# Performance work log

Hardware: AMD Instinct MI355X
Metric: run time of the kernel (lower is better)

## Reference

```python
import jax, jax.numpy as jnp
import numpy as np

B, S, D, H = 2, 2048, 4096, 32
HD = D // H  # 128
HALF = HD // 2  # 64


def setup_inputs() -> dict:
    key = jax.random.key(0)
    ks = jax.random.split(key, 6)
    scale = 1.0 / np.sqrt(D)
    x = jax.random.normal(ks[0], (B, S, D), jnp.float32)
    Wq = jax.random.normal(ks[1], (D, D), jnp.float32) * scale
    Wk = jax.random.normal(ks[2], (D, D), jnp.float32) * scale
    Wv = jax.random.normal(ks[3], (D, D), jnp.float32) * scale
    Wo = jax.random.normal(ks[4], (D, D), jnp.float32) * scale
    # Rotary frequencies: complex freqs of shape (S, HD//2) split into cos/sin
    inv_freq = 1.0 / (10000.0 ** (np.arange(0, HD, 2, dtype=np.float32) / HD))
    angles = np.outer(np.arange(S, dtype=np.float32), inv_freq)  # (S, HALF)
    freq_cos = jnp.asarray(np.cos(angles), jnp.float32)
    freq_sin = jnp.asarray(np.sin(angles), jnp.float32)
    # Additive causal mask (0 on/below diag, large-negative above)
    causal = jnp.tril(jnp.ones((S, S), jnp.bool_))
    mask = jnp.where(causal, 0.0, -1e9).astype(jnp.float32)
    return {"x": x, "Wq": Wq, "Wk": Wk, "Wv": Wv, "Wo": Wo,
            "freq_cos": freq_cos, "freq_sin": freq_sin, "mask": mask,
            "start_position": 0, "n_rep": 1}


def _apply_rope(t, freq_cos, freq_sin):
    # t: [B, S, H, HD]; complex multiply on interleaved (even, odd) pairs
    b, s, h, hd = t.shape
    tr = t.reshape(b, s, h, hd // 2, 2)
    a, c = tr[..., 0], tr[..., 1]
    cos = freq_cos[None, :, None, :]  # [1, S, 1, HALF]
    sin = freq_sin[None, :, None, :]
    out = jnp.stack([a * cos - c * sin, a * sin + c * cos], axis=-1)
    return out.reshape(b, s, h, hd)


def reference(x, Wq, Wk, Wv, Wo, freq_cos, freq_sin, mask, start_position, n_rep):
    b, s, _ = x.shape
    q = (x @ Wq).reshape(b, s, H, HD)
    k = (x @ Wk).reshape(b, s, H, HD)
    v = (x @ Wv).reshape(b, s, H, HD)
    q = _apply_rope(q, freq_cos, freq_sin)
    k = _apply_rope(k, freq_cos, freq_sin)
    if n_rep > 1:  # repeat_kv (identity when n_rep == 1)
        k = jnp.repeat(k, n_rep, axis=2)
        v = jnp.repeat(v, n_rep, axis=2)
    # KV-cache: with start_position=0 and s == max_sequence_length, the
    # cache slice [:, :start_position+s] equals the freshly written k/v.
    scores = jnp.einsum('bqhd,bkhd->bhqk', q, k) / jnp.sqrt(jnp.float32(HD))
    scores = scores + mask  # broadcast [S,S] over [B,H,S,S]
    weights = jax.nn.softmax(scores, axis=-1)
    out = jnp.einsum('bhqk,bkhd->bqhd', weights, v)
    out = out.reshape(b, s, H * HD)
    return out @ Wo
```

## Files before the change

### kernel.cpp

```cpp
#include <hip/hip_runtime.h>
#include <hip/hip_bf16.h>

#define DD 4096
#define MM 4096
#define SS 2048
#define HH 32
#define HDD 128
#define NT 64

typedef unsigned short u16;
typedef unsigned int u32;
typedef __attribute__((ext_vector_type(8))) __bf16 bf16x8;
typedef __attribute__((ext_vector_type(4))) float f32x4;
typedef __attribute__((ext_vector_type(4))) float float4v;
typedef __attribute__((ext_vector_type(8))) unsigned short ushort8;
typedef __attribute__((ext_vector_type(4))) unsigned int uint4v;

__device__ __forceinline__ u16 f2bf(float f) {
  union { float f; unsigned u; } v; v.f = f;
  unsigned u = v.u;
  return (u16)((u + 0x7fffu + ((u >> 16) & 1u)) >> 16);
}
__device__ __forceinline__ float bf2f(u16 s) {
  union { unsigned u; float f; } v; v.u = ((unsigned)s) << 16;
  return v.f;
}
__device__ __forceinline__ f32x4 zero4() { f32x4 z = {0.f, 0.f, 0.f, 0.f}; return z; }

__device__ __forceinline__ void gl_lds16(const u16* g, u16* l) {
  __builtin_amdgcn_global_load_lds((__attribute__((address_space(1))) void*)(g),
                                   (__attribute__((address_space(3))) void*)(l), 16, 0, 0);
}

__device__ __forceinline__ unsigned cvtpk(float lo, float hi) {
  unsigned r;
  asm("v_cvt_pk_bf16_f32 %0, %1, %2" : "=v"(r) : "v"(lo), "v"(hi));
  return r;
}
__device__ __forceinline__ u16 cvt1(float v) {
  unsigned r;
  asm("v_cvt_pk_bf16_f32 %0, %1, %1" : "=v"(r) : "v"(v));
  return (u16)r;
}
__device__ __forceinline__ float exp2a(float x) {
  float r;
  asm("v_exp_f32 %0, %1" : "=v"(r) : "v"(x));
  return r;
}

__global__ __launch_bounds__(256) void k_cvt(const float* __restrict__ in,
                                             u16* __restrict__ out, int n8) {
  int i = blockIdx.x * blockDim.x + threadIdx.x;
  if (i >= n8) return;
  size_t o = (size_t)i * 8;
  float4v a = *(const float4v*)(in + o);
  float4v b = *(const float4v*)(in + o + 4);
  ushort8 v;
  v[0] = f2bf(a[0]); v[1] = f2bf(a[1]); v[2] = f2bf(a[2]); v[3] = f2bf(a[3]);
  v[4] = f2bf(b[0]); v[5] = f2bf(b[1]); v[6] = f2bf(b[2]); v[7] = f2bf(b[3]);
  *(ushort8*)(out + o) = v;
}

__global__ __launch_bounds__(256) void k_wt(const float* __restrict__ W0,
                                            const float* __restrict__ W1,
                                            const float* __restrict__ W2,
                                            const float* __restrict__ W3,
                                            u16* __restrict__ out) {
  const float* W = blockIdx.z == 0 ? W0 : blockIdx.z == 1 ? W1 : blockIdx.z == 2 ? W2 : W3;
  u16* O = out + (size_t)blockIdx.z * DD * DD;
  __shared__ u16 t[64][66];
  int k0 = blockIdx.x * 64, n0 = blockIdx.y * 64;
  int tx = threadIdx.x, ty = threadIdx.y;
#pragma unroll
  for (int i = 0; i < 16; ++i) {
    int kk = ty + i * 4;
    t[tx][kk] = cvt1(W[(size_t)(k0 + kk) * DD + n0 + tx]);
  }
  __syncthreads();
  const int L = ty * 64 + tx;
  const int kx = L & 31, nb = L >> 5;
#pragma unroll
  for (int i = 0; i < 8; ++i) {
    int nn = nb + i * 8;
    u32 pk = *(const u32*)&t[nn][2 * kx];
    *(u32*)&O[(size_t)(n0 + nn) * DD + k0 + 2 * kx] = pk;
  }
}

#define MFMA16(QM, QN)                                                             \
  _Pragma("unroll") for (int kk = 0; kk < 2; ++kk)                                 \
  _Pragma("unroll") for (int mi = 0; mi < 4; ++mi)                                 \
  _Pragma("unroll") for (int ni = 0; ni < 2; ++ni)                                 \
      acc[(QM)*4 + mi][(QN)*2 + ni] = __builtin_amdgcn_mfma_f32_16x16x32_bf16(     \
          af[mi][kk], bf[(QN)*2 + ni][kk], acc[(QM)*4 + mi][(QN)*2 + ni], 0, 0, 0);

#define RDA(BB, QM)                                                                \
  _Pragma("unroll") for (int mi = 0; mi < 4; ++mi)                                 \
  _Pragma("unroll") for (int kk = 0; kk < 2; ++kk)                                 \
      af[mi][kk] = *(const bf16x8*)((const char*)&L[BB][0][0] +                    \
          ((abase + ((QM)*4 + mi) * 2048 + kk * 64) ^ xsw));

#define RDB(BB, QN)                                                                \
  _Pragma("unroll") for (int ni = 0; ni < 2; ++ni)                                 \
  _Pragma("unroll") for (int kk = 0; kk < 2; ++kk)                                 \
      bf[(QN)*2 + ni][kk] = *(const bf16x8*)((const char*)&L[BB][1][0] +           \
          ((bbase + ((QN)*2 + ni) * 2048 + kk * 64) ^ xsw));

#define BAR() __builtin_amdgcn_s_barrier()
#define LGKM0() asm volatile("s_waitcnt lgkmcnt(0)" ::: "memory")
#define PRIO1() __builtin_amdgcn_s_setprio(1)
#define PRIO0() __builtin_amdgcn_s_setprio(0)

template <int MODE>
__global__ __launch_bounds__(512, 2) void k_gemm(const u16* __restrict__ A,
                                                 const u16* __restrict__ Bt,
                                                 void* __restrict__ Cout) {
  __shared__ __align__(16) u16 L[2][2][16384];
  const int tid = threadIdx.x;
  const int wid = tid >> 6, lane = tid & 63;
  const int g = lane >> 4, li = lane & 15;
  const int wr = wid >> 2, wc = wid & 3;

  const int bid = blockIdx.x;
  const int sw = ((bid & 7) << 5) | (bid >> 3);
  const int brow = (sw >> 4) * 256, bcol = (sw & 15) * 256;

  const int xsw = (li & 7) << 4;
  const int abase = (wr * 128 + li) * 128 + g * 16;
  const int bbase = (wc * 64 + li) * 128 + g * 16;

  const int sxy = ((tid >> 3) & 7) << 3;
  const int scol = ((tid * 8) ^ sxy) & 63;
  const int srow0 = tid >> 3;

  auto STAGEH = [&](int t, int mat, int half) {
    if (t >= NT) return;
    const int bb2 = t & 1;
    const u16* G = mat ? Bt : A;
    const int rowbase = (mat ? bcol : brow) + half * 128;
    u16* Ld = &L[bb2][mat][half * 8192 + wid * 512];
    const u16* gsrc = G + (size_t)(rowbase + srow0) * DD + (t << 6) + scol;
    gl_lds16(gsrc, Ld);
    gl_lds16(gsrc + (size_t)64 * DD, Ld + 4096);
  };

  f32x4 acc[8][4];
#pragma unroll
  for (int m = 0; m < 8; ++m)
#pragma unroll
    for (int n = 0; n < 4; ++n) acc[m][n] = zero4();

  bf16x8 af[4][2], bf[4][2];

  STAGEH(0, 0, 0); STAGEH(0, 0, 1); STAGEH(0, 1, 0); STAGEH(0, 1, 1);
  STAGEH(1, 0, 0); STAGEH(1, 1, 0); STAGEH(1, 1, 1);
  asm volatile("s_waitcnt vmcnt(6)" ::: "memory");
  BAR();

  for (int kt = 0; kt < NT; ++kt) {
    const int bb = kt & 1;
    RDA(bb, 0); RDB(bb, 0);
    STAGEH(kt + 1, 0, 1);
    asm volatile("s_waitcnt lgkmcnt(8)" ::: "memory");
    BAR(); LGKM0();
    PRIO1(); MFMA16(0, 0); PRIO0();
    BAR();
    RDB(bb, 1);
    BAR(); LGKM0();
    PRIO1(); MFMA16(0, 1); PRIO0();
    BAR();
    RDA(bb, 1);
    STAGEH(kt + 2, 1, 0);
    BAR(); LGKM0();
    PRIO1(); MFMA16(1, 0); PRIO0();
    BAR();
    STAGEH(kt + 2, 1, 1);
    STAGEH(kt + 2, 0, 0);
    if (kt < NT - 2) {
      asm volatile("s_waitcnt vmcnt(6)" ::: "memory");
    } else {
      asm volatile("s_waitcnt vmcnt(0)" ::: "memory");
    }
    BAR(); LGKM0();
    PRIO1(); MFMA16(1, 1); PRIO0();
    BAR();
  }

#pragma unroll
  for (int m = 0; m < 8; ++m) {
#pragma unroll
    for (int n = 0; n < 4; ++n) {
#pragma unroll
      for (int r = 0; r < 4; ++r) {
        int row = brow + wr * 128 + m * 16 + g * 4 + r;
        int col = bcol + wc * 64 + n * 16 + li;
        float v = acc[m][n][r];
        if (MODE == 0) {
          ((u16*)Cout)[(size_t)row * DD + col] = cvt1(v);
        } else if (MODE == 1) {
          ((u16*)Cout)[((size_t)((row >> 11) << 12) + col) * SS + (row & 2047)] = cvt1(v);
        } else {
          ((float*)Cout)[(size_t)row * DD + col] = v;
        }
      }
    }
  }
}

__global__ __launch_bounds__(256) void k_rope(u16* __restrict__ Q, u16* __restrict__ Kp,
                                              const float* __restrict__ fc,
                                              const float* __restrict__ fs) {
  int idx = blockIdx.x * blockDim.x + threadIdx.x;
  const int n8 = MM * DD / 8;
  const float qsc = idx < n8 ? 0.08838834764831845f * 1.44269504088896340f : 1.0f;
  u16* T = idx < n8 ? Q : Kp;
  int i = idx < n8 ? idx : idx - n8;
  int m = i >> 9;
  int c = (i & 511) * 8;
  int s = m & (SS - 1);
  int i0 = (c & (HDD - 1)) >> 1;
  size_t o = (size_t)m * DD + c;
  ushort8 v = *(ushort8*)(T + o);
  float4v cs = *(const float4v*)(fc + s * 64 + i0);
  float4v sn = *(const float4v*)(fs + s * 64 + i0);
  ushort8 ov;
#pragma unroll
  for (int p = 0; p < 4; ++p) {
    float a = bf2f(v[2 * p]), cc = bf2f(v[2 * p + 1]);
    ov[2 * p]     = cvt1((a * cs[p] - cc * sn[p]) * qsc);
    ov[2 * p + 1] = cvt1((a * sn[p] + cc * cs[p]) * qsc);
  }
  *(ushort8*)(T + o) = ov;
}

__global__ __launch_bounds__(256) void k_attn(const u16* __restrict__ Q,
                                              const u16* __restrict__ K,
                                              const u16* __restrict__ VT,
                                              u16* __restrict__ O) {
  __shared__ __align__(16) u16 Kl[2][32 * 128];
  __shared__ __align__(16) u16 Vl[2][128 * 32];
  __shared__ __align__(16) u16 Pl[4][16 * 32];
  const int bh = blockIdx.x;
  const int qt = 31 - blockIdx.y;
  const int b = bh >> 5, h = bh & 31;
  const int tid = threadIdx.x, w = tid >> 6, lane = tid & 63;
  const int g = lane >> 4, li = lane & 15;

  const u16* Qbase = Q + ((size_t)(b * SS + qt * 64 + w * 16 + li)) * DD + h * HDD;
  const u16* Kbase = K + ((size_t)(b * SS)) * DD + h * HDD;
  const u16* Vbase = VT + ((size_t)bh) * HDD * SS;

  bf16x8 qf[4];
#pragma unroll
  for (int ks = 0; ks < 4; ++ks)
    qf[ks] = *(const bf16x8*)(Qbase + ks * 32 + g * 8);

  f32x4 oa[8];
#pragma unroll
  for (int f = 0; f < 8; ++f) oa[f] = zero4();
  float lrun = 0.f;
  const int wli = w * 16 + li;

  const int krow0 = w * 8 + (lane >> 4);
  const int ksg0 = (lane & 15) ^ (lane >> 4);
  const int ksg1 = (lane & 15) ^ (4 + (lane >> 4));
  const int vdr0 = w * 16 + (lane >> 2);
  const int va0 = (vdr0 * 64 + (lane & 3) * 16) ^ (((vdr0 >> 1) & 7) << 4);
  const int vdr1 = vdr0 + 64;
  const int va1 = (vdr1 * 64 + (lane & 3) * 16) ^ (((vdr1 >> 1) & 7) << 4);

  auto STAGE = [&](int t, int nb) {
    const u16* Kt = Kbase + (size_t)(t * 32) * DD;
    gl_lds16(Kt + (size_t)krow0 * DD + ksg0 * 8, &Kl[nb][(w * 8) * 128]);
    gl_lds16(Kt + (size_t)(krow0 + 4) * DD + ksg1 * 8, &Kl[nb][(w * 8 + 4) * 128]);
    const u16* Vt = Vbase + t * 32;
    gl_lds16(Vt + (size_t)(va0 >> 6) * SS + ((va0 >> 4) & 3) * 8, &Vl[nb][w * 512]);
    gl_lds16(Vt + (size_t)(va1 >> 6) * SS + ((va1 >> 4) & 3) * 8, &Vl[nb][2048 + w * 512]);
  };

  auto TILE = [&](int kt, int cb, int koff) __attribute__((always_inline)) {
    f32x4 sc[2];
    sc[0] = zero4(); sc[1] = zero4();
    PRIO1();
#pragma unroll
    for (int ks = 0; ks < 4; ++ks) {
#pragma unroll
      for (int ktg = 0; ktg < 2; ++ktg) {
        int kr = ktg * 16 + li;
        int off = (kr * 256 + (ks * 32 + g * 8) * 2) ^ ((kr & 7) << 4);
        bf16x8 kf = *(const bf16x8*)((const char*)Kl[cb] + off);
        sc[ktg] = __builtin_amdgcn_mfma_f32_16x16x32_bf16(kf, qf[ks], sc[ktg], 0, 0, 0);
      }
    }
    PRIO0();

    float p[8];
    float su = 0.f;
#pragma unroll
    for (int ktg = 0; ktg < 2; ++ktg) {
#pragma unroll
      for (int r = 0; r < 4; ++r) {
        float s = sc[ktg][r];
        if (koff >= 0 && (koff + ktg * 16 + g * 4 + r > wli)) s = -1e30f;
        float pv = exp2a(s - 16.f);
        p[ktg * 4 + r] = pv;
        su += pv;
      }
    }
    su += __shfl_xor(su, 16);
    su += __shfl_xor(su, 32);
    lrun += su;

    {
      char* Pb = (char*)Pl[w];
      const int swz = ((li >> 1) & 7) << 4;
#pragma unroll
      for (int ktg = 0; ktg < 2; ++ktg) {
#pragma unroll
        for (int j = 0; j < 2; ++j) {
          unsigned pk = cvtpk(p[ktg * 4 + 2 * j], p[ktg * 4 + 2 * j + 1]);
          int off = (li * 64 + ktg * 32 + g * 8 + 4 * j) ^ swz;
          *(unsigned*)(Pb + off) = pk;
        }
      }
    }
    asm volatile("s_waitcnt lgkmcnt(0)" ::: "memory");

    PRIO1();
    {
      int poff = (li * 64 + g * 16) ^ (((li >> 1) & 7) << 4);
      bf16x8 pfrag = *(const bf16x8*)((const char*)Pl[w] + poff);
#pragma unroll
      for (int f = 0; f < 8; ++f) {
        int dr = f * 16 + li;
        int voff = (dr * 64 + g * 16) ^ (((dr >> 1) & 7) << 4);
        bf16x8 vf = *(const bf16x8*)((const char*)Vl[cb] + voff);
        oa[f] = __builtin_amdgcn_mfma_f32_16x16x32_bf16(pfrag, vf, oa[f], 0, 0, 0);
      }
    }
    PRIO0();

    asm volatile("s_waitcnt vmcnt(0)" ::: "memory");
    __syncthreads();
  };

  STAGE(0, 0);
  asm volatile("s_waitcnt vmcnt(0)" ::: "memory");
  __syncthreads();

  for (int i = 0; i < qt; ++i) {
    STAGE(2 * i + 1, 1);
    TILE(2 * i, 0, -1);
    STAGE(2 * i + 2, 0);
    TILE(2 * i + 1, 1, -1);
  }
  STAGE(2 * qt + 1, 1);
  TILE(2 * qt, 0, 0);
  TILE(2 * qt + 1, 1, 32);

  float lv[4];
#pragma unroll
  for (int r = 0; r < 4; ++r) lv[r] = __shfl(lrun, g * 20 + r);
  u16* Ob = O + ((size_t)(b * SS + qt * 64 + w * 16 + g * 4)) * DD + h * HDD;
#pragma unroll
  for (int r = 0; r < 4; ++r) {
    float inv = 1.f / lv[r];
#pragma unroll
    for (int f = 0; f < 8; ++f)
      Ob[(size_t)r * DD + f * 16 + li] = cvt1(oa[f][r] * inv);
  }
}

extern "C" void kernel_launch(void* const* d_in, const int* in_sizes, int n_in,
                              void* d_out, int out_size, void* d_ws, size_t ws_size,
                              hipStream_t stream) {
  (void)in_sizes; (void)n_in; (void)out_size; (void)ws_size;
  const float* x    = (const float*)d_in[0];
  const float* Wq   = (const float*)d_in[1];
  const float* Wk   = (const float*)d_in[2];
  const float* Wv   = (const float*)d_in[3];
  const float* Wo   = (const float*)d_in[4];
  const float* fcos = (const float*)d_in[5];
  const float* fsin = (const float*)d_in[6];

  u16* ws = (u16*)d_ws;
  const size_t MAT = (size_t)4096 * 4096;
  u16* xb    = ws + 0 * MAT;
  u16* wqt   = ws + 1 * MAT;
  u16* wkt   = ws + 2 * MAT;
  u16* wvt   = ws + 3 * MAT;
  u16* wot   = ws + 4 * MAT;
  u16* Qb    = ws + 5 * MAT;
  u16* Kb    = ws + 6 * MAT;
  u16* VTb   = ws + 7 * MAT;
  u16* attnb = ws + 8 * MAT;

  k_cvt<<<dim3(8192), dim3(256), 0, stream>>>(x, xb, (int)(MAT / 8));
  k_wt<<<dim3(64, 64, 4), dim3(64, 4), 0, stream>>>(Wq, Wk, Wv, Wo, wqt);
  k_gemm<0><<<dim3(256), dim3(512), 0, stream>>>(xb, wqt, (void*)Qb);
  k_gemm<0><<<dim3(256), dim3(512), 0, stream>>>(xb, wkt, (void*)Kb);
  k_gemm<1><<<dim3(256), dim3(512), 0, stream>>>(xb, wvt, (void*)VTb);
  k_rope<<<dim3(16384), dim3(256), 0, stream>>>(Qb, Kb, fcos, fsin);
  k_attn<<<dim3(64, 32), dim3(256), 0, stream>>>(Qb, Kb, VTb, attnb);
  k_gemm<2><<<dim3(256), dim3(512), 0, stream>>>(attnb, wot, d_out);
}
```

Measured before the change: 757.0 us.

## Shrink GEMM tile to 128x256 with BK=32 and higher occupancy

Replaces the 256x256x64 GEMM tile, which used a four-phase split MFMA schedule, with a 128x256 tile at K-step 32. The new version has a simpler double-buffered loop and 512 blocks per GEMM launch. LDS and accumulator footprint shrink, so launch_bounds asks for 4 blocks per CU. The aim is better occupancy and latency hiding. The cost is lower arithmetic intensity per tile, twice as many barriers per K, and the loss of the LDS XOR swizzle, which may introduce bank conflicts.

```diff
diff --git a/kernel.cpp b/kernel.cpp
--- a/kernel.cpp
+++ b/kernel.cpp
@@ -6,7 +6,6 @@
 #define SS 2048
 #define HH 32
 #define HDD 128
-#define NT 64
 
 typedef unsigned short u16;
 typedef unsigned int u32;
@@ -87,112 +86,96 @@
   }
 }
 
-#define MFMA16(QM, QN)                                                             \
-  _Pragma("unroll") for (int kk = 0; kk < 2; ++kk)                                 \
-  _Pragma("unroll") for (int mi = 0; mi < 4; ++mi)                                 \
-  _Pragma("unroll") for (int ni = 0; ni < 2; ++ni)                                 \
-      acc[(QM)*4 + mi][(QN)*2 + ni] = __builtin_amdgcn_mfma_f32_16x16x32_bf16(     \
-          af[mi][kk], bf[(QN)*2 + ni][kk], acc[(QM)*4 + mi][(QN)*2 + ni], 0, 0, 0);
-
-#define RDA(BB, QM)                                                                \
-  _Pragma("unroll") for (int mi = 0; mi < 4; ++mi)                                 \
-  _Pragma("unroll") for (int kk = 0; kk < 2; ++kk)                                 \
-      af[mi][kk] = *(const bf16x8*)((const char*)&L[BB][0][0] +                    \
-          ((abase + ((QM)*4 + mi) * 2048 + kk * 64) ^ xsw));
-
-#define RDB(BB, QN)                                                                \
-  _Pragma("unroll") for (int ni = 0; ni < 2; ++ni)                                 \
-  _Pragma("unroll") for (int kk = 0; kk < 2; ++kk)                                 \
-      bf[(QN)*2 + ni][kk] = *(const bf16x8*)((const char*)&L[BB][1][0] +           \
-          ((bbase + ((QN)*2 + ni) * 2048 + kk * 64) ^ xsw));
-
 #define BAR() __builtin_amdgcn_s_barrier()
 #define LGKM0() asm volatile("s_waitcnt lgkmcnt(0)" ::: "memory")
+#define VM3() asm volatile("s_waitcnt vmcnt(3)" ::: "memory")
+#define VM0() asm volatile("s_waitcnt vmcnt(0)" ::: "memory")
 #define PRIO1() __builtin_amdgcn_s_setprio(1)
 #define PRIO0() __builtin_amdgcn_s_setprio(0)
 
+#define GTILE(AP, BP, T, STG, WAIT)                                                \
+  {                                                                                \
+    _Pragma("unroll") for (int mi = 0; mi < 4; ++mi)                               \
+        af[mi] = *(const bf16x8*)((AP) + mi * 1024);                               \
+    _Pragma("unroll") for (int ni = 0; ni < 4; ++ni)                               \
+        bfr[ni] = *(const bf16x8*)((BP) + ni * 1024);                              \
+    LGKM0();                                                                       \
+    BAR();                                                                         \
+    if (STG) {                                                                     \
+      const int k0 = (T + 2) << 5;                                                 \
+      gl_lds16(gA + k0, dA[(T)&1]);                                                \
+      gl_lds16(gB0 + k0, dB0[(T)&1]);                                              \
+      gl_lds16(gB1 + k0, dB1[(T)&1]);                                              \
+    }                                                                              \
+    WAIT();                                                                        \
+    PRIO1();                                                                       \
+    _Pragma("unroll") for (int mi = 0; mi < 4; ++mi)                               \
+    _Pragma("unroll") for (int ni = 0; ni < 4; ++ni)                               \
+        acc[mi][ni] =                                                              \
+            __builtin_amdgcn_mfma_f32_16x16x32_bf16(af[mi], bfr[ni], acc[mi][ni], 0, 0, 0); \
+    PRIO0();                                                                       \
+    BAR();                                                                         \
+  }
+
 template <int MODE>
-__global__ __launch_bounds__(512, 2) void k_gemm(const u16* __restrict__ A,
+__global__ __launch_bounds__(512, 4) void k_gemm(const u16* __restrict__ A,
                                                  const u16* __restrict__ Bt,
                                                  void* __restrict__ Cout) {
-  __shared__ __align__(16) u16 L[2][2][16384];
+  __shared__ __align__(16) u16 LA[2][4096];
+  __shared__ __align__(16) u16 LB[2][8192];
   const int tid = threadIdx.x;
   const int wid = tid >> 6, lane = tid & 63;
   const int g = lane >> 4, li = lane & 15;
   const int wr = wid >> 2, wc = wid & 3;
 
   const int bid = blockIdx.x;
-  const int sw = ((bid & 7) << 5) | (bid >> 3);
-  const int brow = (sw >> 4) * 256, bcol = (sw & 15) * 256;
-
-  const int xsw = (li & 7) << 4;
-  const int abase = (wr * 128 + li) * 128 + g * 16;
-  const int bbase = (wc * 64 + li) * 128 + g * 16;
-
-  const int sxy = ((tid >> 3) & 7) << 3;
-  const int scol = ((tid * 8) ^ sxy) & 63;
-  const int srow0 = tid >> 3;
-
-  auto STAGEH = [&](int t, int mat, int half) {
-    if (t >= NT) return;
-    const int bb2 = t & 1;
-    const u16* G = mat ? Bt : A;
-    const int rowbase = (mat ? bcol : brow) + half * 128;
-    u16* Ld = &L[bb2][mat][half * 8192 + wid * 512];
-    const u16* gsrc = G + (size_t)(rowbase + srow0) * DD + (t << 6) + scol;
-    gl_lds16(gsrc, Ld);
-    gl_lds16(gsrc + (size_t)64 * DD, Ld + 4096);
-  };
-
-  f32x4 acc[8][4];
-#pragma unroll
-  for (int m = 0; m < 8; ++m)
+  const int sw = ((bid & 7) << 6) | (bid >> 3);
+  const int brow = (sw >> 4) * 128, bcol = (sw & 15) * 256;
+
+  const char* LAc = (const char*)&LA[0][0];
+  const char* LBc = (const char*)&LB[0][0];
+  const int aoff = (wr * 64 + li) * 64 + g * 16;
+  const int boff = (wc * 64 + li) * 64 + g * 16;
+  const char* aP[2] = {LAc + aoff, LAc + 8192 + aoff};
+  const char* bP[2] = {LBc + boff, LBc + 16384 + boff};
+
+  const int srow = tid >> 2;
+  const int scol = (tid & 3) * 8;
+  const u16* gA = A + (size_t)(brow + srow) * DD + scol;
+  const u16* gB0 = Bt + (size_t)(bcol + srow) * DD + scol;
+  const u16* gB1 = Bt + (size_t)(bcol + 128 + srow) * DD + scol;
+  u16* dA[2] = {&LA[0][wid * 512], &LA[1][wid * 512]};
+  u16* dB0[2] = {&LB[0][wid * 512], &LB[1][wid * 512]};
+  u16* dB1[2] = {&LB[0][4096 + wid * 512], &LB[1][4096 + wid * 512]};
+
+  f32x4 acc[4][4];
+#pragma unroll
+  for (int m = 0; m < 4; ++m)
 #pragma unroll
     for (int n = 0; n < 4; ++n) acc[m][n] = zero4();
 
-  bf16x8 af[4][2], bf[4][2];
-
-  STAGEH(0, 0, 0); STAGEH(0, 0, 1); STAGEH(0, 1, 0); STAGEH(0, 1, 1);
-  STAGEH(1, 0, 0); STAGEH(1, 1, 0); STAGEH(1, 1, 1);
-  asm volatile("s_waitcnt vmcnt(6)" ::: "memory");
+  bf16x8 af[4], bfr[4];
+
+  gl_lds16(gA, dA[0]); gl_lds16(gB0, dB0[0]); gl_lds16(gB1, dB1[0]);
+  gl_lds16(gA + 32, dA[1]); gl_lds16(gB0 + 32, dB0[1]); gl_lds16(gB1 + 32, dB1[1]);
+  VM3();
   BAR();
 
-  for (int kt = 0; kt < NT; ++kt) {
-    const int bb = kt & 1;
-    RDA(bb, 0); RDB(bb, 0);
-    STAGEH(kt + 1, 0, 1);
-    asm volatile("s_waitcnt lgkmcnt(8)" ::: "memory");
-    BAR(); LGKM0();
-    PRIO1(); MFMA16(0, 0); PRIO0();
-    BAR();
-    RDB(bb, 1);
-    BAR(); LGKM0();
-    PRIO1(); MFMA16(0, 1); PRIO0();
-    BAR();
-    RDA(bb, 1);
-    STAGEH(kt + 2, 1, 0);
-    BAR(); LGKM0();
-    PRIO1(); MFMA16(1, 0); PRIO0();
-    BAR();
-    STAGEH(kt + 2, 1, 1);
-    STAGEH(kt + 2, 0, 0);
-    if (kt < NT - 2) {
-      asm volatile("s_waitcnt vmcnt(6)" ::: "memory");
-    } else {
-      asm volatile("s_waitcnt vmcnt(0)" ::: "memory");
-    }
-    BAR(); LGKM0();
-    PRIO1(); MFMA16(1, 1); PRIO0();
-    BAR();
-  }
-
-#pragma unroll
-  for (int m = 0; m < 8; ++m) {
+  for (int it = 0; it < 63; ++it) {
+    const int t0 = 2 * it;
+    GTILE(aP[0], bP[0], t0, 1, VM3);
+    GTILE(aP[1], bP[1], t0 + 1, 1, VM3);
+  }
+  GTILE(aP[0], bP[0], 126, 0, VM0);
+  GTILE(aP[1], bP[1], 127, 0, VM0);
+
+#pragma unroll
+  for (int m = 0; m < 4; ++m) {
 #pragma unroll
     for (int n = 0; n < 4; ++n) {
 #pragma unroll
       for (int r = 0; r < 4; ++r) {
-        int row = brow + wr * 128 + m * 16 + g * 4 + r;
+        int row = brow + wr * 64 + m * 16 + g * 4 + r;
         int col = bcol + wc * 64 + n * 16 + li;
         float v = acc[m][n][r];
         if (MODE == 0) {
@@ -397,10 +380,10 @@
 
   k_cvt<<<dim3(8192), dim3(256), 0, stream>>>(x, xb, (int)(MAT / 8));
   k_wt<<<dim3(64, 64, 4), dim3(64, 4), 0, stream>>>(Wq, Wk, Wv, Wo, wqt);
-  k_gemm<0><<<dim3(256), dim3(512), 0, stream>>>(xb, wqt, (void*)Qb);
-  k_gemm<0><<<dim3(256), dim3(512), 0, stream>>>(xb, wkt, (void*)Kb);
-  k_gemm<1><<<dim3(256), dim3(512), 0, stream>>>(xb, wvt, (void*)VTb);
+  k_gemm<0><<<dim3(512), dim3(512), 0, stream>>>(xb, wqt, (void*)Qb);
+  k_gemm<0><<<dim3(512), dim3(512), 0, stream>>>(xb, wkt, (void*)Kb);
+  k_gemm<1><<<dim3(512), dim3(512), 0, stream>>>(xb, wvt, (void*)VTb);
   k_rope<<<dim3(16384), dim3(256), 0, stream>>>(Qb, Kb, fcos, fsin);
   k_attn<<<dim3(64, 32), dim3(256), 0, stream>>>(Qb, Kb, VTb, attnb);
-  k_gemm<2><<<dim3(256), dim3(512), 0, stream>>>(attnb, wot, d_out);
-}
+  k_gemm<2><<<dim3(512), dim3(512), 0, stream>>>(attnb, wot, d_out);
+}
```

Result: slower. 840.8 us (+11.1%).

## Merge Q/K/V projections into one launch and precompute LDS pointers in GEMM

Applied to the files above, without the earlier changes.

The three separate QKV GEMM launches are replaced by one 768-block kernel that picks the projection from the block index, relying on the contiguous layout of wqt/wkt/wvt and Qb/Kb/VTb in the workspace. The K loop is unrolled by two so LDS read pointers and global/LDS staging addresses are precomputed constants, not recomputed per iteration. The intent is to fill the GPU better with more concurrent blocks, remove launch gaps and tail effects between projections, and cut address arithmetic. The projection-interleaving swizzle changes L2 locality across projections, and the larger unrolled loop may raise register pressure or code size.

```diff
diff --git a/kernel.cpp b/kernel.cpp
--- a/kernel.cpp
+++ b/kernel.cpp
@@ -87,6 +87,14 @@
   }
 }
 
+#define BAR() __builtin_amdgcn_s_barrier()
+#define LGKM0() asm volatile("s_waitcnt lgkmcnt(0)" ::: "memory")
+#define LGKM8() asm volatile("s_waitcnt lgkmcnt(8)" ::: "memory")
+#define VM6() asm volatile("s_waitcnt vmcnt(6)" ::: "memory")
+#define VM0() asm volatile("s_waitcnt vmcnt(0)" ::: "memory")
+#define PRIO1() __builtin_amdgcn_s_setprio(1)
+#define PRIO0() __builtin_amdgcn_s_setprio(0)
+
 #define MFMA16(QM, QN)                                                             \
   _Pragma("unroll") for (int kk = 0; kk < 2; ++kk)                                 \
   _Pragma("unroll") for (int mi = 0; mi < 4; ++mi)                                 \
@@ -94,97 +102,165 @@
       acc[(QM)*4 + mi][(QN)*2 + ni] = __builtin_amdgcn_mfma_f32_16x16x32_bf16(     \
           af[mi][kk], bf[(QN)*2 + ni][kk], acc[(QM)*4 + mi][(QN)*2 + ni], 0, 0, 0);
 
-#define RDA(BB, QM)                                                                \
-  _Pragma("unroll") for (int mi = 0; mi < 4; ++mi)                                 \
-  _Pragma("unroll") for (int kk = 0; kk < 2; ++kk)                                 \
-      af[mi][kk] = *(const bf16x8*)((const char*)&L[BB][0][0] +                    \
-          ((abase + ((QM)*4 + mi) * 2048 + kk * 64) ^ xsw));
-
-#define RDB(BB, QN)                                                                \
-  _Pragma("unroll") for (int ni = 0; ni < 2; ++ni)                                 \
-  _Pragma("unroll") for (int kk = 0; kk < 2; ++kk)                                 \
-      bf[(QN)*2 + ni][kk] = *(const bf16x8*)((const char*)&L[BB][1][0] +           \
-          ((bbase + ((QN)*2 + ni) * 2048 + kk * 64) ^ xsw));
-
-#define BAR() __builtin_amdgcn_s_barrier()
-#define LGKM0() asm volatile("s_waitcnt lgkmcnt(0)" ::: "memory")
-#define PRIO1() __builtin_amdgcn_s_setprio(1)
-#define PRIO0() __builtin_amdgcn_s_setprio(0)
-
-template <int MODE>
-__global__ __launch_bounds__(512, 2) void k_gemm(const u16* __restrict__ A,
-                                                 const u16* __restrict__ Bt,
-                                                 void* __restrict__ Cout) {
-  __shared__ __align__(16) u16 L[2][2][16384];
-  const int tid = threadIdx.x;
-  const int wid = tid >> 6, lane = tid & 63;
-  const int g = lane >> 4, li = lane & 15;
-  const int wr = wid >> 2, wc = wid & 3;
-
+#define RDA2(P0, P1, QM)                                                           \
+  _Pragma("unroll") for (int mi = 0; mi < 4; ++mi) {                               \
+    af[mi][0] = *(const bf16x8*)((P0) + ((QM)*4 + mi) * 2048);                     \
+    af[mi][1] = *(const bf16x8*)((P1) + ((QM)*4 + mi) * 2048);                     \
+  }
+
+#define RDB2(P0, P1, QN)                                                           \
+  _Pragma("unroll") for (int ni = 0; ni < 2; ++ni) {                               \
+    bf[(QN)*2 + ni][0] = *(const bf16x8*)((P0) + ((QN)*2 + ni) * 2048);            \
+    bf[(QN)*2 + ni][1] = *(const bf16x8*)((P1) + ((QN)*2 + ni) * 2048);            \
+  }
+
+#define GEMM_KLOOP()                                                               \
+  SH(gA0, dA0b0); SH(gA1, dA1b0); SH(gB0, dB0b0); SH(gB1, dB1b0);                  \
+  SH(gA0 + 64, dA0b1); SH(gB0 + 64, dB0b1); SH(gB1 + 64, dB1b1);                   \
+  VM6();                                                                           \
+  BAR();                                                                           \
+  for (int it = 0; it < 31; ++it) {                                                \
+    const u16* a0 = gA0 + it * 128;                                                \
+    const u16* a1 = gA1 + it * 128;                                                \
+    const u16* b0 = gB0 + it * 128;                                                \
+    const u16* b1 = gB1 + it * 128;                                                \
+    RDA2(aP00, aP01, 0); RDB2(bP00, bP01, 0);                                      \
+    SH(a1 + 64, dA1b1);                                                            \
+    LGKM8();                                                                       \
+    BAR(); LGKM0();                                                                \
+    PRIO1(); MFMA16(0, 0); PRIO0();                                                \
+    BAR();                                                                         \
+    RDB2(bP00, bP01, 1);                                                           \
+    BAR(); LGKM0();                                                                \
+    PRIO1(); MFMA16(0, 1); PRIO0();                                                \
+    BAR();                                                                         \
+    RDA2(aP00, aP01, 1);                                                           \
+    SH(b0 + 128, dB0b0);                                                           \
+    BAR(); LGKM0();                                                                \
+    PRIO1(); MFMA16(1, 0); PRIO0();                                                \
+    BAR();                                                                         \
+    SH(b1 + 128, dB1b0);                                                           \
+    SH(a0 + 128, dA0b0);                                                           \
+    VM6();                                                                         \
+    BAR(); LGKM0();                                                                \
+    PRIO1(); MFMA16(1, 1); PRIO0();                                                \
+    BAR();                                                                         \
+    RDA2(aP10, aP11, 0); RDB2(bP10, bP11, 0);                                      \
+    SH(a1 + 128, dA1b0);                                                           \
+    LGKM8();                                                                       \
+    BAR(); LGKM0();                                                                \
+    PRIO1(); MFMA16(0, 0); PRIO0();                                                \
+    BAR();                                                                         \
+    RDB2(bP10, bP11, 1);                                                           \
+    BAR(); LGKM0();                                                                \
+    PRIO1(); MFMA16(0, 1); PRIO0();                                                \
+    BAR();                                                                         \
+    RDA2(aP10, aP11, 1);                                                           \
+    SH(b0 + 192, dB0b1);                                                           \
+    BAR(); LGKM0();                                                                \
+    PRIO1(); MFMA16(1, 0); PRIO0();                                                \
+    BAR();                                                                         \
+    SH(b1 + 192, dB1b1);                                                           \
+    SH(a0 + 192, dA0b1);                                                           \
+    VM6();                                                                         \
+    BAR(); LGKM0();                                                                \
+    PRIO1(); MFMA16(1, 1); PRIO0();                                                \
+    BAR();                                                                         \
+  }                                                                                \
+  {                                                                                \
+    const u16* a1 = gA1 + 31 * 128;                                                \
+    RDA2(aP00, aP01, 0); RDB2(bP00, bP01, 0);                                      \
+    SH(a1 + 64, dA1b1);                                                            \
+    LGKM8();                                                                       \
+    BAR(); LGKM0();                                                                \
+    PRIO1(); MFMA16(0, 0); PRIO0();                                                \
+    BAR();                                                                         \
+    RDB2(bP00, bP01, 1);                                                           \
+    BAR(); LGKM0();                                                                \
+    PRIO1(); MFMA16(0, 1); PRIO0();                                                \
+    BAR();                                                                         \
+    RDA2(aP00, aP01, 1);                                                           \
+    BAR(); LGKM0();                                                                \
+    PRIO1(); MFMA16(1, 0); PRIO0();                                                \
+    BAR();                                                                         \
+    VM0();                                                                         \
+    BAR(); LGKM0();                                                                \
+    PRIO1(); MFMA16(1, 1); PRIO0();                                                \
+    BAR();                                                                         \
+  }                                                                                \
+  {                                                                                \
+    RDA2(aP10, aP11, 0); RDB2(bP10, bP11, 0);                                      \
+    BAR(); LGKM0();                                                                \
+    PRIO1(); MFMA16(0, 0); PRIO0();                                                \
+    BAR();                                                                         \
+    RDB2(bP10, bP11, 1);                                                           \
+    BAR(); LGKM0();                                                                \
+    PRIO1(); MFMA16(0, 1); PRIO0();                                                \
+    BAR();                                                                         \
+    RDA2(aP10, aP11, 1);                                                           \
+    BAR(); LGKM0();                                                                \
+    PRIO1(); MFMA16(1, 0); PRIO0();                                                \
+    BAR();                                                                         \
+    BAR(); LGKM0();                                                                \
+    PRIO1(); MFMA16(1, 1); PRIO0();                                                \
+    BAR();                                                                         \
+  }
+
+#define GEMM_SETUP()                                                               \
+  __shared__ __align__(16) u16 L[2][2][16384];                                     \
+  const int tid = threadIdx.x;                                                     \
+  const int wid = tid >> 6, lane = tid & 63;                                       \
+  const int g = lane >> 4, li = lane & 15;                                         \
+  const int wr = wid >> 2, wc = wid & 3;                                           \
+  const int xsw = (li & 7) << 4;                                                   \
+  const int abase = (wr * 128 + li) * 128 + g * 16;                                \
+  const int bbase = (wc * 64 + li) * 128 + g * 16;                                 \
+  const char* Lc = (const char*)&L[0][0][0];                                       \
+  const char* aP00 = Lc + ((abase) ^ xsw);                                         \
+  const char* aP01 = Lc + ((abase + 64) ^ xsw);                                    \
+  const char* aP10 = Lc + 65536 + ((abase) ^ xsw);                                 \
+  const char* aP11 = Lc + 65536 + ((abase + 64) ^ xsw);                            \
+  const char* bP00 = Lc + 32768 + ((bbase) ^ xsw);                                 \
+  const char* bP01 = Lc + 32768 + ((bbase + 64) ^ xsw);                            \
+  const char* bP10 = Lc + 98304 + ((bbase) ^ xsw);                                 \
+  const char* bP11 = Lc + 98304 + ((bbase + 64) ^ xsw);                            \
+  const int sxy = ((tid >> 3) & 7) << 3;                                           \
+  const int scol = ((tid * 8) ^ sxy) & 63;                                         \
+  const int srow0 = tid >> 3;                                                      \
+  const u16* gA0 = A + (size_t)(brow + srow0) * DD + scol;                         \
+  const u16* gA1 = A + (size_t)(brow + 128 + srow0) * DD + scol;                   \
+  const u16* gB0 = Bt + (size_t)(bcol + srow0) * DD + scol;                        \
+  const u16* gB1 = Bt + (size_t)(bcol + 128 + srow0) * DD + scol;                  \
+  u16* dA0b0 = &L[0][0][wid * 512];                                                \
+  u16* dA1b0 = &L[0][0][8192 + wid * 512];                                         \
+  u16* dB0b0 = &L[0][1][wid * 512];                                                \
+  u16* dB1b0 = &L[0][1][8192 + wid * 512];                                         \
+  u16* dA0b1 = &L[1][0][wid * 512];                                                \
+  u16* dA1b1 = &L[1][0][8192 + wid * 512];                                         \
+  u16* dB0b1 = &L[1][1][wid * 512];                                                \
+  u16* dB1b1 = &L[1][1][8192 + wid * 512];                                         \
+  auto SH = [&](const u16* gsrc, u16* ld) {                                        \
+    gl_lds16(gsrc, ld);                                                            \
+    gl_lds16(gsrc + (size_t)64 * DD, ld + 4096);                                   \
+  };                                                                               \
+  f32x4 acc[8][4];                                                                 \
+  _Pragma("unroll") for (int m = 0; m < 8; ++m)                                    \
+  _Pragma("unroll") for (int n = 0; n < 4; ++n) acc[m][n] = zero4();               \
+  bf16x8 af[4][2], bf[4][2];
+
+__global__ __launch_bounds__(512, 2) void k_gemm_qkv(const u16* __restrict__ A,
+                                                     const u16* __restrict__ Wt,
+                                                     u16* __restrict__ Out) {
   const int bid = blockIdx.x;
-  const int sw = ((bid & 7) << 5) | (bid >> 3);
-  const int brow = (sw >> 4) * 256, bcol = (sw & 15) * 256;
-
-  const int xsw = (li & 7) << 4;
-  const int abase = (wr * 128 + li) * 128 + g * 16;
-  const int bbase = (wc * 64 + li) * 128 + g * 16;
-
-  const int sxy = ((tid >> 3) & 7) << 3;
-  const int scol = ((tid * 8) ^ sxy) & 63;
-  const int srow0 = tid >> 3;
-
-  auto STAGEH = [&](int t, int mat, int half) {
-    if (t >= NT) return;
-    const int bb2 = t & 1;
-    const u16* G = mat ? Bt : A;
-    const int rowbase = (mat ? bcol : brow) + half * 128;
-    u16* Ld = &L[bb2][mat][half * 8192 + wid * 512];
-    const u16* gsrc = G + (size_t)(rowbase + srow0) * DD + (t << 6) + scol;
-    gl_lds16(gsrc, Ld);
-    gl_lds16(gsrc + (size_t)64 * DD, Ld + 4096);
-  };
-
-  f32x4 acc[8][4];
-#pragma unroll
-  for (int m = 0; m < 8; ++m)
-#pragma unroll
-    for (int n = 0; n < 4; ++n) acc[m][n] = zero4();
-
-  bf16x8 af[4][2], bf[4][2];
-
-  STAGEH(0, 0, 0); STAGEH(0, 0, 1); STAGEH(0, 1, 0); STAGEH(0, 1, 1);
-  STAGEH(1, 0, 0); STAGEH(1, 1, 0); STAGEH(1, 1, 1);
-  asm volatile("s_waitcnt vmcnt(6)" ::: "memory");
-  BAR();
-
-  for (int kt = 0; kt < NT; ++kt) {
-    const int bb = kt & 1;
-    RDA(bb, 0); RDB(bb, 0);
-    STAGEH(kt + 1, 0, 1);
-    asm volatile("s_waitcnt lgkmcnt(8)" ::: "memory");
-    BAR(); LGKM0();
-    PRIO1(); MFMA16(0, 0); PRIO0();
-    BAR();
-    RDB(bb, 1);
-    BAR(); LGKM0();
-    PRIO1(); MFMA16(0, 1); PRIO0();
-    BAR();
-    RDA(bb, 1);
-    STAGEH(kt + 2, 1, 0);
-    BAR(); LGKM0();
-    PRIO1(); MFMA16(1, 0); PRIO0();
-    BAR();
-    STAGEH(kt + 2, 1, 1);
-    STAGEH(kt + 2, 0, 0);
-    if (kt < NT - 2) {
-      asm volatile("s_waitcnt vmcnt(6)" ::: "memory");
-    } else {
-      asm volatile("s_waitcnt vmcnt(0)" ::: "memory");
-    }
-    BAR(); LGKM0();
-    PRIO1(); MFMA16(1, 1); PRIO0();
-    BAR();
-  }
+  const int sw = (bid & 7) * 96 + (bid >> 3);
+  const int proj = sw >> 8;
+  const int rem = sw & 255;
+  const int brow = (rem >> 4) * 256, bcol = (rem & 15) * 256;
+  const u16* Bt = Wt + (size_t)proj * DD * DD;
+  u16* Cout = Out + (size_t)proj * DD * DD;
+
+  GEMM_SETUP();
+  GEMM_KLOOP();
 
 #pragma unroll
   for (int m = 0; m < 8; ++m) {
@@ -195,13 +271,35 @@
         int row = brow + wr * 128 + m * 16 + g * 4 + r;
         int col = bcol + wc * 64 + n * 16 + li;
         float v = acc[m][n][r];
-        if (MODE == 0) {
-          ((u16*)Cout)[(size_t)row * DD + col] = cvt1(v);
-        } else if (MODE == 1) {
-          ((u16*)Cout)[((size_t)((row >> 11) << 12) + col) * SS + (row & 2047)] = cvt1(v);
+        if (proj != 2) {
+          Cout[(size_t)row * DD + col] = cvt1(v);
         } else {
-          ((float*)Cout)[(size_t)row * DD + col] = v;
+          Cout[((size_t)((row >> 11) << 12) + col) * SS + (row & 2047)] = cvt1(v);
         }
+      }
+    }
+  }
+}
+
+__global__ __launch_bounds__(512, 2) void k_gemm_o(const u16* __restrict__ A,
+                                                   const u16* __restrict__ Bt,
+                                                   float* __restrict__ Cout) {
+  const int bid = blockIdx.x;
+  const int sw = ((bid & 7) << 5) | (bid >> 3);
+  const int brow = (sw >> 4) * 256, bcol = (sw & 15) * 256;
+
+  GEMM_SETUP();
+  GEMM_KLOOP();
+
+#pragma unroll
+  for (int m = 0; m < 8; ++m) {
+#pragma unroll
+    for (int n = 0; n < 4; ++n) {
+#pragma unroll
+      for (int r = 0; r < 4; ++r) {
+        int row = brow + wr * 128 + m * 16 + g * 4 + r;
+        int col = bcol + wc * 64 + n * 16 + li;
+        Cout[(size_t)row * DD + col] = acc[m][n][r];
       }
     }
   }
@@ -387,8 +485,6 @@
   const size_t MAT = (size_t)4096 * 4096;
   u16* xb    = ws + 0 * MAT;
   u16* wqt   = ws + 1 * MAT;
-  u16* wkt   = ws + 2 * MAT;
-  u16* wvt   = ws + 3 * MAT;
   u16* wot   = ws + 4 * MAT;
   u16* Qb    = ws + 5 * MAT;
   u16* Kb    = ws + 6 * MAT;
@@ -397,10 +493,8 @@
 
   k_cvt<<<dim3(8192), dim3(256), 0, stream>>>(x, xb, (int)(MAT / 8));
   k_wt<<<dim3(64, 64, 4), dim3(64, 4), 0, stream>>>(Wq, Wk, Wv, Wo, wqt);
-  k_gemm<0><<<dim3(256), dim3(512), 0, stream>>>(xb, wqt, (void*)Qb);
-  k_gemm<0><<<dim3(256), dim3(512), 0, stream>>>(xb, wkt, (void*)Kb);
-  k_gemm<1><<<dim3(256), dim3(512), 0, stream>>>(xb, wvt, (void*)VTb);
+  k_gemm_qkv<<<dim3(768), dim3(512), 0, stream>>>(xb, wqt, Qb);
   k_rope<<<dim3(16384), dim3(256), 0, stream>>>(Qb, Kb, fcos, fsin);
   k_attn<<<dim3(64, 32), dim3(256), 0, stream>>>(Qb, Kb, VTb, attnb);
-  k_gemm<2><<<dim3(256), dim3(512), 0, stream>>>(attnb, wot, d_out);
-}
+  k_gemm_o<<<dim3(256), dim3(512), 0, stream>>>(attnb, wot, (float*)d_out);
+}
```

New measurement: 786.2 us. 3.9% more time.
